# Kernel tuning notes

Hardware: AMD Instinct MI355X
Metric: run time of the kernel (lower is better)

## Reference

```python
import jax, jax.numpy as jnp
import numpy as np

N_NODES = 100_000
N_EDGES = 1_200_000
D = 64


def setup_inputs() -> dict:
    key = jax.random.key(0)
    k1, k2, k3, k4, k5 = jax.random.split(key, 5)
    feat = jax.random.normal(k1, (N_NODES, D), dtype=jnp.float32)
    feat_0 = jax.random.normal(k2, (N_NODES, D), dtype=jnp.float32)
    std = 1.0 / np.sqrt(D)  # reset_parameters: uniform(-std, std), std = 1/sqrt(out_size)
    weight = jax.random.uniform(k3, (D, D), dtype=jnp.float32, minval=-std, maxval=std)
    src = jax.random.randint(k4, (N_EDGES,), 0, N_NODES, dtype=jnp.int32)
    dst = jax.random.randint(k5, (N_EDGES,), 0, N_NODES, dtype=jnp.int32)
    return {
        "feat": feat,
        "feat_0": feat_0,
        "weight": weight,
        "src": src,
        "dst": dst,
        "alpha": jnp.float32(0.1),
        "lamda": jnp.float32(0.5),
        "layer": 1,
    }


def reference(feat, feat_0, weight, src, dst, alpha, lamda, layer):
    # beta = log(lamda / layer + 1)
    beta = jnp.log(lamda / layer + 1.0)
    # in-degrees from destination endpoints, clamped at 1 (as in DGL path)
    degs = jax.ops.segment_sum(
        jnp.ones_like(dst, dtype=feat.dtype), dst, num_segments=N_NODES
    )
    norm = jnp.maximum(degs, 1.0) ** -0.5  # [N]
    norm = norm[:, None]  # [N, 1]
    # symmetric degree-normalized SpMM: D^{-1/2} A D^{-1/2} X via copy_u + sum
    h = feat * norm
    h = jax.ops.segment_sum(h[src], dst, num_segments=N_NODES)  # scatter-add over edges
    h = h * norm
    # GCNII combination: initial residual + identity mapping
    feat_sum = h * (1.0 - alpha) + feat_0 * alpha
    rst = (1.0 - beta) * feat_sum + beta * (feat_sum @ weight)
    return rst
```

## Files before the change

kernel.cpp:

```cpp
#include <hip/hip_runtime.h>

#define DDIM 64
#define MAXNS 2048
#define PART_TPB 256
#define PART_EPT 16
#define PART_EPB (PART_TPB * PART_EPT)

__device__ __forceinline__ float atomAddF(float* p, float v) {
    return unsafeAtomicAdd(p, v);
}


__global__ void slice_count_kernel(const int* __restrict__ dst, int* __restrict__ sliceCnt,
                                   int nE, int NS) {
    __shared__ int lh[MAXNS];
    int t = threadIdx.x;
    int blockBase = blockIdx.x * PART_EPB;
    for (int i = t; i < NS; i += PART_TPB) lh[i] = 0;
    __syncthreads();
    #pragma unroll
    for (int c = 0; c < 4; ++c) {
        int e0 = blockBase + (c * PART_TPB + t) * 4;
        if (e0 + 3 < nE) {
            int4 b = *(const int4*)(dst + e0);
            atomicAdd(&lh[b.x >> 8], 1); atomicAdd(&lh[b.y >> 8], 1);
            atomicAdd(&lh[b.z >> 8], 1); atomicAdd(&lh[b.w >> 8], 1);
        } else {
            for (int j = 0; j < 4; ++j) {
                int e = e0 + j;
                if (e < nE) atomicAdd(&lh[dst[e] >> 8], 1);
            }
        }
    }
    __syncthreads();
    for (int i = t; i < NS; i += PART_TPB)
        if (lh[i]) atomicAdd(&sliceCnt[i], lh[i]);
}

__global__ void slice_scan_wp_kernel(int* __restrict__ scnt, int* __restrict__ sbase,
                                     int NS, int nE,
                                     const float* __restrict__ W, const float* __restrict__ lamda_p,
                                     const int* __restrict__ layer_p, float* __restrict__ Wp) {
    __shared__ int sdata[512];
    int t = threadIdx.x;
    int base = t * 4;
    int v[4];
    #pragma unroll
    for (int j = 0; j < 4; ++j) {
        int idx = base + j;
        v[j] = (idx < NS) ? scnt[idx] : 0;
    }
    int local = v[0] + v[1] + v[2] + v[3];
    sdata[t] = local;
    __syncthreads();
    for (int off = 1; off < 512; off <<= 1) {
        int y = (t >= off) ? sdata[t - off] : 0;
        __syncthreads();
        sdata[t] += y;
        __syncthreads();
    }
    int run = sdata[t] - local;
    #pragma unroll
    for (int j = 0; j < 4; ++j) {
        int idx = base + j;
        if (idx < NS) { sbase[idx] = run; scnt[idx] = run; }
        run += v[j];
    }
    if (t == 0) sbase[NS] = nE;

    float lam = lamda_p[0];
    int lb = layer_p[0];
    float layerf = (lb > 0 && lb < (1 << 23)) ? (float)lb : __int_as_float(lb);
    float beta = logf(lam / layerf + 1.0f);
    for (int i = t; i < DDIM * DDIM; i += 512) {
        int k = i >> 6, d = i & 63;
        float w = beta * W[i];
        if (k == d) w += (1.0f - beta);
        Wp[i] = w;
    }
}

__global__ void partition_kernel(const int* __restrict__ src, const int* __restrict__ dst,
                                 int* __restrict__ cursor, unsigned* __restrict__ staging,
                                 int nE, int NS) {
    __shared__ int lh[MAXNS];
    __shared__ int lbase[MAXNS];
    int t = threadIdx.x;
    int blockBase = blockIdx.x * PART_EPB;
    for (int i = t; i < NS; i += PART_TPB) lh[i] = 0;
    __syncthreads();

    int se[PART_EPT]; int de[PART_EPT];
    #pragma unroll
    for (int c = 0; c < 4; ++c) {
        int e0 = blockBase + (c * PART_TPB + t) * 4;
        if (e0 + 3 < nE) {
            int4 a = *(const int4*)(src + e0);
            int4 b = *(const int4*)(dst + e0);
            se[4*c+0] = a.x; se[4*c+1] = a.y; se[4*c+2] = a.z; se[4*c+3] = a.w;
            de[4*c+0] = b.x; de[4*c+1] = b.y; de[4*c+2] = b.z; de[4*c+3] = b.w;
        } else {
            #pragma unroll
            for (int j = 0; j < 4; ++j) {
                int e = e0 + j;
                se[4*c+j] = (e < nE) ? src[e] : 0;
                de[4*c+j] = (e < nE) ? dst[e] : -1;
            }
        }
    }
    #pragma unroll
    for (int k = 0; k < PART_EPT; ++k)
        if (de[k] >= 0) atomicAdd(&lh[de[k] >> 8], 1);
    __syncthreads();
    for (int i = t; i < NS; i += PART_TPB) {
        int c = lh[i];
        if (c) lbase[i] = atomicAdd(&cursor[i], c);
        lh[i] = 0;
    }
    __syncthreads();
    #pragma unroll
    for (int k = 0; k < PART_EPT; ++k) {
        int d = de[k];
        if (d >= 0) {
            int sl = d >> 8;
            int off = atomicAdd(&lh[sl], 1);
            staging[lbase[sl] + off] = ((unsigned)se[k] << 8) | (unsigned)(d & 255);
        }
    }
}

__global__ void bin_fill_kernel(const unsigned* __restrict__ staging, const int* __restrict__ sbase,
                                int* __restrict__ degI, float* __restrict__ normv,
                                int* __restrict__ row_end, int* __restrict__ eidx, int nN) {
    __shared__ int cnt[256];
    __shared__ int pos[256];
    int s = blockIdx.x;
    int t = threadIdx.x;
    int b0 = sbase[s], b1 = sbase[s + 1];
    cnt[t] = 0;
    __syncthreads();
    for (int j = b0 + t; j < b1; j += 256) {
        unsigned p = staging[j];
        atomicAdd(&cnt[p & 255], 1);
    }
    __syncthreads();
    int c = cnt[t];
    pos[t] = c;
    __syncthreads();
    for (int off = 1; off < 256; off <<= 1) {
        int y = (t >= off) ? pos[t - off] : 0;
        __syncthreads();
        pos[t] += y;
        __syncthreads();
    }
    int inc = pos[t];
    int exc = inc - c;
    int node = (s << 8) + t;
    if (node < nN) {
        degI[node] = c;
        normv[node] = rsqrtf(fmaxf((float)c, 1.0f));
        row_end[node] = b0 + inc;
    }
    pos[t] = b0 + exc;
    __syncthreads();
    for (int j = b0 + t; j < b1; j += 256) {
        unsigned p = staging[j];
        int q = atomicAdd(&pos[p & 255], 1);
        eidx[q] = (int)(p >> 8);
    }
}

__global__ void scale_kernel(const float4* __restrict__ feat4, const float* __restrict__ normv,
                             float4* __restrict__ featS4, int nN) {
    int b = blockIdx.x, t = threadIdx.x;
    int node = b * 16 + (t >> 4);
    int r = t & 15;
    if (node < nN) {
        float nv = normv[node];
        float4 v = feat4[(size_t)node * 16 + r];
        v.x *= nv; v.y *= nv; v.z *= nv; v.w *= nv;
        featS4[(size_t)node * 16 + r] = v;
    }
}


__global__ void deg_int_kernel(const int* __restrict__ dst, int* __restrict__ degI, int nE) {
    int i = blockIdx.x * blockDim.x + threadIdx.x;
    int base = i * 4;
    if (base + 3 < nE) {
        int4 d = *(const int4*)(dst + base);
        atomicAdd(&degI[d.x], 1); atomicAdd(&degI[d.y], 1);
        atomicAdd(&degI[d.z], 1); atomicAdd(&degI[d.w], 1);
    } else {
        for (int j = base; j < nE; ++j) atomicAdd(&degI[dst[j]], 1);
    }
}

#define SCAN_BLOCK 256
#define SCAN_CHUNK 1024

__global__ void scan1_kernel(const int* __restrict__ degI, int* __restrict__ row_start,
                             float* __restrict__ normv, int* __restrict__ blockSums, int nN) {
    __shared__ int sdata[SCAN_BLOCK];
    int t = threadIdx.x;
    int base = blockIdx.x * SCAN_CHUNK + t * 4;
    int v[4];
    #pragma unroll
    for (int j = 0; j < 4; ++j) {
        int idx = base + j;
        v[j] = (idx < nN) ? degI[idx] : 0;
    }
    int local = v[0] + v[1] + v[2] + v[3];
    sdata[t] = local;
    __syncthreads();
    for (int off = 1; off < SCAN_BLOCK; off <<= 1) {
        int y = (t >= off) ? sdata[t - off] : 0;
        __syncthreads();
        sdata[t] += y;
        __syncthreads();
    }
    int inc = sdata[t];
    int exc = inc - local;
    if (t == SCAN_BLOCK - 1) blockSums[blockIdx.x] = inc;
    int run = exc;
    #pragma unroll
    for (int j = 0; j < 4; ++j) {
        int idx = base + j;
        if (idx < nN) {
            row_start[idx] = run;
            normv[idx] = rsqrtf(fmaxf((float)v[j], 1.0f));
        }
        run += v[j];
    }
}

__global__ void scan2_wp_kernel(int* __restrict__ blockSums, int nb,
                                const float* __restrict__ W, const float* __restrict__ lamda_p,
                                const int* __restrict__ layer_p, float* __restrict__ Wp) {
    __shared__ int sdata[SCAN_BLOCK];
    int t = threadIdx.x;
    int v = (t < nb) ? blockSums[t] : 0;
    sdata[t] = v;
    __syncthreads();
    for (int off = 1; off < SCAN_BLOCK; off <<= 1) {
        int y = (t >= off) ? sdata[t - off] : 0;
        __syncthreads();
        sdata[t] += y;
        __syncthreads();
    }
    if (t < nb) blockSums[t] = sdata[t] - v;

    float lam = lamda_p[0];
    int lb = layer_p[0];
    float layerf = (lb > 0 && lb < (1 << 23)) ? (float)lb : __int_as_float(lb);
    float beta = logf(lam / layerf + 1.0f);
    for (int i = t; i < DDIM * DDIM; i += SCAN_BLOCK) {
        int k = i >> 6, d = i & 63;
        float w = beta * W[i];
        if (k == d) w += (1.0f - beta);
        Wp[i] = w;
    }
}

__global__ void scan3_scale_kernel(int* __restrict__ row_start, const int* __restrict__ blockSums,
                                   const float4* __restrict__ feat4, const float* __restrict__ normv,
                                   float4* __restrict__ featS4, int nN) {
    int b = blockIdx.x, t = threadIdx.x;
    int node = b * 16 + (t >> 4);
    int r = t & 15;
    if (node < nN) {
        float nv = normv[node];
        float4 v = feat4[(size_t)node * 16 + r];
        v.x *= nv; v.y *= nv; v.z *= nv; v.w *= nv;
        featS4[(size_t)node * 16 + r] = v;
    }
    if (t < 16) {
        int n2 = b * 16 + t;
        if (n2 < nN) row_start[n2] += blockSums[n2 >> 10];
    }
}

__global__ void scan3_kernel(int* __restrict__ row_start, const int* __restrict__ blockSums, int nN) {
    int i = blockIdx.x * blockDim.x + threadIdx.x;
    if (i < nN) row_start[i] += blockSums[i >> 10];
}

__global__ void fill_kernel(const int* __restrict__ src, const int* __restrict__ dst,
                            int* __restrict__ row_start, int* __restrict__ eidx, int nE) {
    int i = blockIdx.x * blockDim.x + threadIdx.x;
    int base = i * 4;
    if (base + 3 < nE) {
        int4 s = *(const int4*)(src + base);
        int4 d = *(const int4*)(dst + base);
        eidx[atomicAdd(&row_start[d.x], 1)] = s.x;
        eidx[atomicAdd(&row_start[d.y], 1)] = s.y;
        eidx[atomicAdd(&row_start[d.z], 1)] = s.z;
        eidx[atomicAdd(&row_start[d.w], 1)] = s.w;
    } else {
        for (int j = base; j < nE; ++j) {
            int tt = dst[j];
            int p = atomicAdd(&row_start[tt], 1);
            eidx[p] = src[j];
        }
    }
}

template<bool SCALED>
__global__ void gather_kernel(const float4* __restrict__ featv, const float4* __restrict__ feat04,
                              const float* __restrict__ normv, const int* __restrict__ degI,
                              const int* __restrict__ row_end, const int* __restrict__ eidx,
                              const float* __restrict__ Wp, const float* __restrict__ alpha_p,
                              float4* __restrict__ out4, int nN) {
    __shared__ float4 sW[DDIM * 16];
    const float4* Wp4 = (const float4*)Wp;
    for (int i = threadIdx.x; i < DDIM * 16; i += blockDim.x) {
        sW[(i & ~15) | ((i & 15) ^ ((i >> 8) & 3))] = Wp4[i];
    }
    __syncthreads();

    int lane = threadIdx.x & 63;
    int w = threadIdx.x >> 6;
    int g = lane >> 4;
    int r = lane & 15;
    int n = blockIdx.x * 4 + w;
    if (n >= nN) return;

    int end = row_end[n];
    int deg = degI[n];
    int start = end - deg;

    float4 acc = make_float4(0.f, 0.f, 0.f, 0.f);

    for (int j0 = start; j0 < end; j0 += 64) {
        int m = end - j0; if (m > 64) m = 64;
        int sIdx = 0;
        float nv = 1.0f;
        if (lane < m) {
            sIdx = eidx[j0 + lane];
            if (!SCALED) nv = normv[sIdx];
        }
        int nt = (m + 3) >> 2;
        int t = 0;
        for (; t + 2 <= nt; t += 2) {
            int e0 = 4 * t + g, e1 = e0 + 4;
            int s0 = __shfl(sIdx, e0, 64);
            int s1 = __shfl(sIdx, e1, 64);
            float ns0 = SCALED ? 1.0f : __shfl(nv, e0, 64);
            float ns1 = SCALED ? 1.0f : __shfl(nv, e1, 64);
            float4 a = featv[(size_t)s0 * 16 + r];
            float4 b = featv[(size_t)s1 * 16 + r];
            float w0 = (e0 < m) ? ns0 : 0.0f;
            float w1 = (e1 < m) ? ns1 : 0.0f;
            acc.x = fmaf(a.x, w0, acc.x); acc.y = fmaf(a.y, w0, acc.y);
            acc.z = fmaf(a.z, w0, acc.z); acc.w = fmaf(a.w, w0, acc.w);
            acc.x = fmaf(b.x, w1, acc.x); acc.y = fmaf(b.y, w1, acc.y);
            acc.z = fmaf(b.z, w1, acc.z); acc.w = fmaf(b.w, w1, acc.w);
        }
        for (; t < nt; ++t) {
            int e = 4 * t + g;
            int s = __shfl(sIdx, e, 64);
            float ns = SCALED ? 1.0f : __shfl(nv, e, 64);
            float4 a = featv[(size_t)s * 16 + r];
            float w0 = (e < m) ? ns : 0.0f;
            acc.x = fmaf(a.x, w0, acc.x); acc.y = fmaf(a.y, w0, acc.y);
            acc.z = fmaf(a.z, w0, acc.z); acc.w = fmaf(a.w, w0, acc.w);
        }
    }

    acc.x += __shfl_xor(acc.x, 16, 64); acc.y += __shfl_xor(acc.y, 16, 64);
    acc.z += __shfl_xor(acc.z, 16, 64); acc.w += __shfl_xor(acc.w, 16, 64);
    acc.x += __shfl_xor(acc.x, 32, 64); acc.y += __shfl_xor(acc.y, 32, 64);
    acc.z += __shfl_xor(acc.z, 32, 64); acc.w += __shfl_xor(acc.w, 32, 64);

    float alpha = alpha_p[0];
    float sn = normv[n] * (1.0f - alpha);
    float4 f0 = feat04[(size_t)n * 16 + r];
    float4 fs;
    fs.x = fmaf(acc.x, sn, f0.x * alpha);
    fs.y = fmaf(acc.y, sn, f0.y * alpha);
    fs.z = fmaf(acc.z, sn, f0.z * alpha);
    fs.w = fmaf(acc.w, sn, f0.w * alpha);

    float4 res = make_float4(0.f, 0.f, 0.f, 0.f);
    #pragma unroll
    for (int kk = 0; kk < 16; ++kk) {
        int srcLane = 4 * g + (kk >> 2);
        float fscomp = ((kk & 3) == 0) ? fs.x : ((kk & 3) == 1) ? fs.y
                     : ((kk & 3) == 2) ? fs.z : fs.w;
        float fsk = __shfl(fscomp, srcLane, 64);
        float4 wv = sW[(16 * g + kk) * 16 + (r ^ g)];
        res.x = fmaf(fsk, wv.x, res.x);
        res.y = fmaf(fsk, wv.y, res.y);
        res.z = fmaf(fsk, wv.z, res.z);
        res.w = fmaf(fsk, wv.w, res.w);
    }
    res.x += __shfl_xor(res.x, 16, 64); res.y += __shfl_xor(res.y, 16, 64);
    res.z += __shfl_xor(res.z, 16, 64); res.w += __shfl_xor(res.w, 16, 64);
    res.x += __shfl_xor(res.x, 32, 64); res.y += __shfl_xor(res.y, 32, 64);
    res.z += __shfl_xor(res.z, 32, 64); res.w += __shfl_xor(res.w, 32, 64);

    if (g == 0) out4[(size_t)n * 16 + r] = res;
}


__global__ void deg_kernel(const int* __restrict__ dst, float* __restrict__ degs, int nE) {
    int i = blockIdx.x * blockDim.x + threadIdx.x;
    if (i < nE) atomAddF(&degs[dst[i]], 1.0f);
}

__global__ void norm_kernel(float* degs, int nN) {
    int i = blockIdx.x * blockDim.x + threadIdx.x;
    if (i < nN) degs[i] = rsqrtf(fmaxf(degs[i], 1.0f));
}

__global__ void wp_kernel(const float* __restrict__ W, const float* __restrict__ lamda_p,
                          const int* __restrict__ layer_p, float* __restrict__ Wp) {
    int i = blockIdx.x * blockDim.x + threadIdx.x;
    if (i < DDIM * DDIM) {
        float lam = lamda_p[0];
        int lb = layer_p[0];
        float layerf = (lb > 0 && lb < (1 << 23)) ? (float)lb : __int_as_float(lb);
        float beta = logf(lam / layerf + 1.0f);
        int k = i >> 6, d = i & 63;
        float w = beta * W[i];
        if (k == d) w += (1.0f - beta);
        Wp[i] = w;
    }
}

__global__ void scatter_kernel(const float* __restrict__ feat, const float* __restrict__ norm,
                               const int* __restrict__ src, const int* __restrict__ dst,
                               float* __restrict__ accum, int nE) {
    long long gid = (long long)blockIdx.x * blockDim.x + threadIdx.x;
    int e = (int)(gid >> 6);
    int d = (int)(gid & 63);
    if (e < nE) {
        int s = src[e];
        int t = dst[e];
        float v = feat[(size_t)s * DDIM + d] * norm[s];
        atomAddF(&accum[(size_t)t * DDIM + d], v);
    }
}

__global__ void final_kernel(float* __restrict__ out, const float* __restrict__ feat0,
                             const float* __restrict__ norm, const float* __restrict__ Wp,
                             const float* __restrict__ alpha_p, int nN) {
    __shared__ float sW[DDIM * DDIM];
    for (int i = threadIdx.x; i < DDIM * DDIM; i += blockDim.x) sW[i] = Wp[i];
    __syncthreads();
    float alpha = alpha_p[0];
    int lane = threadIdx.x & 63;
    int w = threadIdx.x >> 6;
    int wavesPerBlock = blockDim.x >> 6;
    int nGroups = (nN + wavesPerBlock - 1) / wavesPerBlock;
    for (int gi = blockIdx.x; gi < nGroups; gi += gridDim.x) {
        int n = gi * wavesPerBlock + w;
        bool valid = n < nN;
        float fs = 0.0f;
        if (valid) {
            fs = out[(size_t)n * DDIM + lane] * norm[n] * (1.0f - alpha)
               + feat0[(size_t)n * DDIM + lane] * alpha;
        }
        float acc = 0.0f;
        #pragma unroll
        for (int k = 0; k < DDIM; ++k) {
            float fsk = __shfl(fs, k, 64);
            acc = fmaf(fsk, sW[k * DDIM + lane], acc);
        }
        if (valid) out[(size_t)n * DDIM + lane] = acc;
    }
}


static inline size_t align256(size_t x) { return (x + 255) & ~(size_t)255; }

extern "C" void kernel_launch(void* const* d_in, const int* in_sizes, int n_in,
                              void* d_out, int out_size, void* d_ws, size_t ws_size,
                              hipStream_t stream) {
    const float* feat  = (const float*)d_in[0];
    const float* feat0 = (const float*)d_in[1];
    const float* W     = (const float*)d_in[2];
    const int*   src   = (const int*)d_in[3];
    const int*   dst   = (const int*)d_in[4];
    const float* alpha = (const float*)d_in[5];
    const float* lamda = (const float*)d_in[6];
    const int*   layer = (const int*)d_in[7];
    float* out = (float*)d_out;

    int nN = in_sizes[0] / DDIM;
    int nE = in_sizes[3];
    int NS = (nN + 255) >> 8;
    int nb = (nN + SCAN_CHUNK - 1) / SCAN_CHUNK;

    size_t off = 0;
    size_t o_degI  = off; off += align256((size_t)nN * 4);
    size_t o_norm  = off; off += align256((size_t)nN * 4);
    size_t o_rowe  = off; off += align256((size_t)nN * 4);
    size_t o_sbase = off; off += align256((size_t)(NS + 1) * 4);
    size_t o_scnt  = off; off += align256((size_t)NS * 4);
    size_t o_wp    = off; off += align256((size_t)DDIM * DDIM * 4);
    size_t o_eidx  = off; off += align256((size_t)nE * 4);
    size_t base_sz = off;
    size_t o_featS = off; off += align256((size_t)nN * DDIM * 4);
    size_t need_t1 = off;
    size_t o_stag2 = base_sz;
    size_t need_t2 = base_sz + align256((size_t)nE * 4);

    bool newok = (NS >= 1 && NS <= MAXNS && nN <= (1 << 24));
    bool t1ok  = newok && ws_size >= need_t1 && ((size_t)nE * 4 <= (size_t)nN * DDIM * 4);
    bool t2ok  = newok && ws_size >= need_t2;

    if (t1ok || t2ok) {
        int*      degI  = (int*)  ((char*)d_ws + o_degI);
        float*    normv = (float*)((char*)d_ws + o_norm);
        int*      rowe  = (int*)  ((char*)d_ws + o_rowe);
        int*      sbase = (int*)  ((char*)d_ws + o_sbase);
        int*      scnt  = (int*)  ((char*)d_ws + o_scnt);
        float*    Wp    = (float*)((char*)d_ws + o_wp);
        int*      eidx  = (int*)  ((char*)d_ws + o_eidx);
        unsigned* stag  = (unsigned*)((char*)d_ws + (t1ok ? o_featS : o_stag2));
        float*    featS = (float*)((char*)d_ws + o_featS);

        hipMemsetAsync(scnt, 0, (size_t)NS * 4, stream);
        int pblocks = (nE + PART_EPB - 1) / PART_EPB;
        if (pblocks < 1) pblocks = 1;
        slice_count_kernel<<<pblocks, PART_TPB, 0, stream>>>(dst, scnt, nE, NS);
        slice_scan_wp_kernel<<<1, 512, 0, stream>>>(scnt, sbase, NS, nE, W, lamda, layer, Wp);
        partition_kernel<<<pblocks, PART_TPB, 0, stream>>>(src, dst, scnt, stag, nE, NS);
        bin_fill_kernel<<<NS, 256, 0, stream>>>(stag, sbase, degI, normv, rowe, eidx, nN);

        int gblocks = (nN + 3) / 4;
        if (t1ok) {
            scale_kernel<<<(nN + 15) / 16, 256, 0, stream>>>(
                (const float4*)feat, normv, (float4*)featS, nN);
            gather_kernel<true><<<gblocks, 256, 0, stream>>>(
                (const float4*)featS, (const float4*)feat0, normv, degI, rowe, eidx,
                Wp, alpha, (float4*)out, nN);
        } else {
            gather_kernel<false><<<gblocks, 256, 0, stream>>>(
                (const float4*)feat, (const float4*)feat0, normv, degI, rowe, eidx,
                Wp, alpha, (float4*)out, nN);
        }
        return;
    }

    off = 0;
    size_t f_degI = off;      off += align256((size_t)nN * 4);
    size_t f_norm = off;      off += align256((size_t)nN * 4);
    size_t f_rows = off;      off += align256((size_t)nN * 4);
    size_t f_bsum = off;      off += align256((size_t)nb * 4);
    size_t f_wp   = off;      off += align256((size_t)DDIM * DDIM * 4);
    size_t f_eidx = off;      off += align256((size_t)nE * 4);
    size_t need_csr = off;
    size_t f_featS = off;     off += align256((size_t)nN * DDIM * 4);
    size_t need_full = off;

    if (ws_size >= need_csr && nb <= SCAN_BLOCK) {
        int*   degI  = (int*)  ((char*)d_ws + f_degI);
        float* normv = (float*)((char*)d_ws + f_norm);
        int*   rows  = (int*)  ((char*)d_ws + f_rows);
        int*   bsum  = (int*)  ((char*)d_ws + f_bsum);
        float* Wp    = (float*)((char*)d_ws + f_wp);
        int*   eidx  = (int*)  ((char*)d_ws + f_eidx);
        bool scaled = (ws_size >= need_full);
        float* featS = (float*)((char*)d_ws + f_featS);

        hipMemsetAsync(degI, 0, (size_t)nN * 4, stream);
        int e4blocks = ((nE + 3) / 4 + 255) / 256;
        deg_int_kernel<<<e4blocks, 256, 0, stream>>>(dst, degI, nE);
        scan1_kernel<<<nb, SCAN_BLOCK, 0, stream>>>(degI, rows, normv, bsum, nN);
        scan2_wp_kernel<<<1, SCAN_BLOCK, 0, stream>>>(bsum, nb, W, lamda, layer, Wp);
        if (scaled) {
            scan3_scale_kernel<<<(nN + 15) / 16, 256, 0, stream>>>(
                rows, bsum, (const float4*)feat, normv, (float4*)featS, nN);
        } else {
            scan3_kernel<<<(nN + 255) / 256, 256, 0, stream>>>(rows, bsum, nN);
        }
        fill_kernel<<<e4blocks, 256, 0, stream>>>(src, dst, rows, eidx, nE);

        int gblocks = (nN + 3) / 4;
        if (scaled) {
            gather_kernel<true><<<gblocks, 256, 0, stream>>>(
                (const float4*)featS, (const float4*)feat0, normv, degI, rows, eidx,
                Wp, alpha, (float4*)out, nN);
        } else {
            gather_kernel<false><<<gblocks, 256, 0, stream>>>(
                (const float4*)feat, (const float4*)feat0, normv, degI, rows, eidx,
                Wp, alpha, (float4*)out, nN);
        }
    } else {
        float* degs = (float*)d_ws;
        size_t degs_bytes_al = align256((size_t)nN * 4);
        float* Wp = (float*)((char*)d_ws + degs_bytes_al);

        hipMemsetAsync(out, 0, (size_t)out_size * sizeof(float), stream);
        hipMemsetAsync(degs, 0, (size_t)nN * sizeof(float), stream);

        deg_kernel<<<(nE + 255) / 256, 256, 0, stream>>>(dst, degs, nE);
        norm_kernel<<<(nN + 255) / 256, 256, 0, stream>>>(degs, nN);
        wp_kernel<<<(DDIM * DDIM + 255) / 256, 256, 0, stream>>>(W, lamda, layer, Wp);

        long long tot = (long long)nE * DDIM;
        int sblocks = (int)((tot + 255) / 256);
        scatter_kernel<<<sblocks, 256, 0, stream>>>(feat, degs, src, dst, out, nE);
        final_kernel<<<2048, 256, 0, stream>>>(out, feat0, degs, Wp, alpha, nN);
    }
}
```

Baseline: 135.1 us.

## Store pre-scaled features in fp16 and make gather grid-stride persistent

```diff
diff --git a/kernel.cpp b/kernel.cpp
--- a/kernel.cpp
+++ b/kernel.cpp
@@ -1,4 +1,5 @@
 #include <hip/hip_runtime.h>
+#include <hip/hip_fp16.h>
 
 #define DDIM 64
 #define MAXNS 2048
@@ -171,15 +172,19 @@
 }
 
 __global__ void scale_kernel(const float4* __restrict__ feat4, const float* __restrict__ normv,
-                             float4* __restrict__ featS4, int nN) {
+                             uint2* __restrict__ featS2, int nN) {
     int b = blockIdx.x, t = threadIdx.x;
     int node = b * 16 + (t >> 4);
     int r = t & 15;
     if (node < nN) {
         float nv = normv[node];
         float4 v = feat4[(size_t)node * 16 + r];
-        v.x *= nv; v.y *= nv; v.z *= nv; v.w *= nv;
-        featS4[(size_t)node * 16 + r] = v;
+        __half2 h0 = __floats2half2_rn(v.x * nv, v.y * nv);
+        __half2 h1 = __floats2half2_rn(v.z * nv, v.w * nv);
+        uint2 u;
+        u.x = *(unsigned*)&h0;
+        u.y = *(unsigned*)&h1;
+        featS2[(size_t)node * 16 + r] = u;
     }
 }
 
@@ -264,15 +269,19 @@
 
 __global__ void scan3_scale_kernel(int* __restrict__ row_start, const int* __restrict__ blockSums,
                                    const float4* __restrict__ feat4, const float* __restrict__ normv,
-                                   float4* __restrict__ featS4, int nN) {
+                                   uint2* __restrict__ featS2, int nN) {
     int b = blockIdx.x, t = threadIdx.x;
     int node = b * 16 + (t >> 4);
     int r = t & 15;
     if (node < nN) {
         float nv = normv[node];
         float4 v = feat4[(size_t)node * 16 + r];
-        v.x *= nv; v.y *= nv; v.z *= nv; v.w *= nv;
-        featS4[(size_t)node * 16 + r] = v;
+        __half2 h0 = __floats2half2_rn(v.x * nv, v.y * nv);
+        __half2 h1 = __floats2half2_rn(v.z * nv, v.w * nv);
+        uint2 u;
+        u.x = *(unsigned*)&h0;
+        u.y = *(unsigned*)&h1;
+        featS2[(size_t)node * 16 + r] = u;
     }
     if (t < 16) {
         int n2 = b * 16 + t;
@@ -305,8 +314,8 @@
     }
 }
 
-template<bool SCALED>
-__global__ void gather_kernel(const float4* __restrict__ featv, const float4* __restrict__ feat04,
+template<bool HALF>
+__global__ void gather_kernel(const void* __restrict__ featv_, const float4* __restrict__ feat04,
                               const float* __restrict__ normv, const int* __restrict__ degI,
                               const int* __restrict__ row_end, const int* __restrict__ eidx,
                               const float* __restrict__ Wp, const float* __restrict__ alpha_p,
@@ -318,88 +327,114 @@
     }
     __syncthreads();
 
+    const float4* featF = (const float4*)featv_;
+    const uint2*  featH = (const uint2*)featv_;
+
     int lane = threadIdx.x & 63;
     int w = threadIdx.x >> 6;
     int g = lane >> 4;
     int r = lane & 15;
-    int n = blockIdx.x * 4 + w;
-    if (n >= nN) return;
-
-    int end = row_end[n];
-    int deg = degI[n];
-    int start = end - deg;
-
-    float4 acc = make_float4(0.f, 0.f, 0.f, 0.f);
-
-    for (int j0 = start; j0 < end; j0 += 64) {
-        int m = end - j0; if (m > 64) m = 64;
-        int sIdx = 0;
-        float nv = 1.0f;
-        if (lane < m) {
-            sIdx = eidx[j0 + lane];
-            if (!SCALED) nv = normv[sIdx];
-        }
-        int nt = (m + 3) >> 2;
-        int t = 0;
-        for (; t + 2 <= nt; t += 2) {
-            int e0 = 4 * t + g, e1 = e0 + 4;
-            int s0 = __shfl(sIdx, e0, 64);
-            int s1 = __shfl(sIdx, e1, 64);
-            float ns0 = SCALED ? 1.0f : __shfl(nv, e0, 64);
-            float ns1 = SCALED ? 1.0f : __shfl(nv, e1, 64);
-            float4 a = featv[(size_t)s0 * 16 + r];
-            float4 b = featv[(size_t)s1 * 16 + r];
-            float w0 = (e0 < m) ? ns0 : 0.0f;
-            float w1 = (e1 < m) ? ns1 : 0.0f;
-            acc.x = fmaf(a.x, w0, acc.x); acc.y = fmaf(a.y, w0, acc.y);
-            acc.z = fmaf(a.z, w0, acc.z); acc.w = fmaf(a.w, w0, acc.w);
-            acc.x = fmaf(b.x, w1, acc.x); acc.y = fmaf(b.y, w1, acc.y);
-            acc.z = fmaf(b.z, w1, acc.z); acc.w = fmaf(b.w, w1, acc.w);
-        }
-        for (; t < nt; ++t) {
-            int e = 4 * t + g;
-            int s = __shfl(sIdx, e, 64);
-            float ns = SCALED ? 1.0f : __shfl(nv, e, 64);
-            float4 a = featv[(size_t)s * 16 + r];
-            float w0 = (e < m) ? ns : 0.0f;
-            acc.x = fmaf(a.x, w0, acc.x); acc.y = fmaf(a.y, w0, acc.y);
-            acc.z = fmaf(a.z, w0, acc.z); acc.w = fmaf(a.w, w0, acc.w);
-        }
-    }
-
-    acc.x += __shfl_xor(acc.x, 16, 64); acc.y += __shfl_xor(acc.y, 16, 64);
-    acc.z += __shfl_xor(acc.z, 16, 64); acc.w += __shfl_xor(acc.w, 16, 64);
-    acc.x += __shfl_xor(acc.x, 32, 64); acc.y += __shfl_xor(acc.y, 32, 64);
-    acc.z += __shfl_xor(acc.z, 32, 64); acc.w += __shfl_xor(acc.w, 32, 64);
-
     float alpha = alpha_p[0];
-    float sn = normv[n] * (1.0f - alpha);
-    float4 f0 = feat04[(size_t)n * 16 + r];
-    float4 fs;
-    fs.x = fmaf(acc.x, sn, f0.x * alpha);
-    fs.y = fmaf(acc.y, sn, f0.y * alpha);
-    fs.z = fmaf(acc.z, sn, f0.z * alpha);
-    fs.w = fmaf(acc.w, sn, f0.w * alpha);
-
-    float4 res = make_float4(0.f, 0.f, 0.f, 0.f);
-    #pragma unroll
-    for (int kk = 0; kk < 16; ++kk) {
-        int srcLane = 4 * g + (kk >> 2);
-        float fscomp = ((kk & 3) == 0) ? fs.x : ((kk & 3) == 1) ? fs.y
-                     : ((kk & 3) == 2) ? fs.z : fs.w;
-        float fsk = __shfl(fscomp, srcLane, 64);
-        float4 wv = sW[(16 * g + kk) * 16 + (r ^ g)];
-        res.x = fmaf(fsk, wv.x, res.x);
-        res.y = fmaf(fsk, wv.y, res.y);
-        res.z = fmaf(fsk, wv.z, res.z);
-        res.w = fmaf(fsk, wv.w, res.w);
-    }
-    res.x += __shfl_xor(res.x, 16, 64); res.y += __shfl_xor(res.y, 16, 64);
-    res.z += __shfl_xor(res.z, 16, 64); res.w += __shfl_xor(res.w, 16, 64);
-    res.x += __shfl_xor(res.x, 32, 64); res.y += __shfl_xor(res.y, 32, 64);
-    res.z += __shfl_xor(res.z, 32, 64); res.w += __shfl_xor(res.w, 32, 64);
-
-    if (g == 0) out4[(size_t)n * 16 + r] = res;
+
+    for (int n = blockIdx.x * 4 + w; n < nN; n += gridDim.x * 4) {
+        int end = row_end[n];
+        int deg = degI[n];
+        int start = end - deg;
+
+        float4 acc = make_float4(0.f, 0.f, 0.f, 0.f);
+
+        for (int j0 = start; j0 < end; j0 += 64) {
+            int m = end - j0; if (m > 64) m = 64;
+            int sIdx = 0;
+            float nv = 1.0f;
+            if (lane < m) {
+                sIdx = eidx[j0 + lane];
+                if (!HALF) nv = normv[sIdx];
+            }
+            int nt = (m + 3) >> 2;
+            int t = 0;
+            for (; t + 2 <= nt; t += 2) {
+                int e0 = 4 * t + g, e1 = e0 + 4;
+                int s0 = __shfl(sIdx, e0, 64);
+                int s1 = __shfl(sIdx, e1, 64);
+                float w0 = (e0 < m) ? 1.0f : 0.0f;
+                float w1 = (e1 < m) ? 1.0f : 0.0f;
+                if (HALF) {
+                    uint2 ua = featH[(size_t)s0 * 16 + r];
+                    uint2 ub = featH[(size_t)s1 * 16 + r];
+                    float2 a0 = __half22float2(*(const __half2*)&ua.x);
+                    float2 a1 = __half22float2(*(const __half2*)&ua.y);
+                    float2 b0 = __half22float2(*(const __half2*)&ub.x);
+                    float2 b1 = __half22float2(*(const __half2*)&ub.y);
+                    acc.x = fmaf(a0.x, w0, acc.x); acc.y = fmaf(a0.y, w0, acc.y);
+                    acc.z = fmaf(a1.x, w0, acc.z); acc.w = fmaf(a1.y, w0, acc.w);
+                    acc.x = fmaf(b0.x, w1, acc.x); acc.y = fmaf(b0.y, w1, acc.y);
+                    acc.z = fmaf(b1.x, w1, acc.z); acc.w = fmaf(b1.y, w1, acc.w);
+                } else {
+                    float ns0 = __shfl(nv, e0, 64);
+                    float ns1 = __shfl(nv, e1, 64);
+                    w0 *= ns0; w1 *= ns1;
+                    float4 a = featF[(size_t)s0 * 16 + r];
+                    float4 b = featF[(size_t)s1 * 16 + r];
+                    acc.x = fmaf(a.x, w0, acc.x); acc.y = fmaf(a.y, w0, acc.y);
+                    acc.z = fmaf(a.z, w0, acc.z); acc.w = fmaf(a.w, w0, acc.w);
+                    acc.x = fmaf(b.x, w1, acc.x); acc.y = fmaf(b.y, w1, acc.y);
+                    acc.z = fmaf(b.z, w1, acc.z); acc.w = fmaf(b.w, w1, acc.w);
+                }
+            }
+            for (; t < nt; ++t) {
+                int e = 4 * t + g;
+                int s = __shfl(sIdx, e, 64);
+                float w0 = (e < m) ? 1.0f : 0.0f;
+                if (HALF) {
+                    uint2 ua = featH[(size_t)s * 16 + r];
+                    float2 a0 = __half22float2(*(const __half2*)&ua.x);
+                    float2 a1 = __half22float2(*(const __half2*)&ua.y);
+                    acc.x = fmaf(a0.x, w0, acc.x); acc.y = fmaf(a0.y, w0, acc.y);
+                    acc.z = fmaf(a1.x, w0, acc.z); acc.w = fmaf(a1.y, w0, acc.w);
+                } else {
+                    float ns = __shfl(nv, e, 64);
+                    w0 *= ns;
+                    float4 a = featF[(size_t)s * 16 + r];
+                    acc.x = fmaf(a.x, w0, acc.x); acc.y = fmaf(a.y, w0, acc.y);
+                    acc.z = fmaf(a.z, w0, acc.z); acc.w = fmaf(a.w, w0, acc.w);
+                }
+            }
+        }
+
+        acc.x += __shfl_xor(acc.x, 16, 64); acc.y += __shfl_xor(acc.y, 16, 64);
+        acc.z += __shfl_xor(acc.z, 16, 64); acc.w += __shfl_xor(acc.w, 16, 64);
+        acc.x += __shfl_xor(acc.x, 32, 64); acc.y += __shfl_xor(acc.y, 32, 64);
+        acc.z += __shfl_xor(acc.z, 32, 64); acc.w += __shfl_xor(acc.w, 32, 64);
+
+        float sn = normv[n] * (1.0f - alpha);
+        float4 f0 = feat04[(size_t)n * 16 + r];
+        float4 fs;
+        fs.x = fmaf(acc.x, sn, f0.x * alpha);
+        fs.y = fmaf(acc.y, sn, f0.y * alpha);
+        fs.z = fmaf(acc.z, sn, f0.z * alpha);
+        fs.w = fmaf(acc.w, sn, f0.w * alpha);
+
+        float4 res = make_float4(0.f, 0.f, 0.f, 0.f);
+        #pragma unroll
+        for (int kk = 0; kk < 16; ++kk) {
+            int srcLane = 4 * g + (kk >> 2);
+            float fscomp = ((kk & 3) == 0) ? fs.x : ((kk & 3) == 1) ? fs.y
+                         : ((kk & 3) == 2) ? fs.z : fs.w;
+            float fsk = __shfl(fscomp, srcLane, 64);
+            float4 wv = sW[(16 * g + kk) * 16 + (r ^ g)];
+            res.x = fmaf(fsk, wv.x, res.x);
+            res.y = fmaf(fsk, wv.y, res.y);
+            res.z = fmaf(fsk, wv.z, res.z);
+            res.w = fmaf(fsk, wv.w, res.w);
+        }
+        res.x += __shfl_xor(res.x, 16, 64); res.y += __shfl_xor(res.y, 16, 64);
+        res.z += __shfl_xor(res.z, 16, 64); res.w += __shfl_xor(res.w, 16, 64);
+        res.x += __shfl_xor(res.x, 32, 64); res.y += __shfl_xor(res.y, 32, 64);
+        res.z += __shfl_xor(res.z, 32, 64); res.w += __shfl_xor(res.w, 32, 64);
+
+        if (g == 0) out4[(size_t)n * 16 + r] = res;
+    }
 }
 
 
@@ -501,13 +536,13 @@
     size_t o_wp    = off; off += align256((size_t)DDIM * DDIM * 4);
     size_t o_eidx  = off; off += align256((size_t)nE * 4);
     size_t base_sz = off;
-    size_t o_featS = off; off += align256((size_t)nN * DDIM * 4);
+    size_t o_featS = off; off += align256((size_t)nN * DDIM * 2);
     size_t need_t1 = off;
     size_t o_stag2 = base_sz;
     size_t need_t2 = base_sz + align256((size_t)nE * 4);
 
-    bool newok = (NS >= 1 && NS <= MAXNS && nN <= (1 << 24));
-    bool t1ok  = newok && ws_size >= need_t1 && ((size_t)nE * 4 <= (size_t)nN * DDIM * 4);
+    bool newok = (NS >= 1 && NS <= MAXNS && nN <= (1 << 23));
+    bool t1ok  = newok && ws_size >= need_t1 && ((size_t)nE * 4 <= (size_t)nN * DDIM * 2);
     bool t2ok  = newok && ws_size >= need_t2;
 
     if (t1ok || t2ok) {
@@ -530,15 +565,16 @@
         bin_fill_kernel<<<NS, 256, 0, stream>>>(stag, sbase, degI, normv, rowe, eidx, nN);
 
         int gblocks = (nN + 3) / 4;
+        if (gblocks > 4096) gblocks = 4096;
         if (t1ok) {
             scale_kernel<<<(nN + 15) / 16, 256, 0, stream>>>(
-                (const float4*)feat, normv, (float4*)featS, nN);
+                (const float4*)feat, normv, (uint2*)featS, nN);
             gather_kernel<true><<<gblocks, 256, 0, stream>>>(
-                (const float4*)featS, (const float4*)feat0, normv, degI, rowe, eidx,
+                (const void*)featS, (const float4*)feat0, normv, degI, rowe, eidx,
                 Wp, alpha, (float4*)out, nN);
         } else {
             gather_kernel<false><<<gblocks, 256, 0, stream>>>(
-                (const float4*)feat, (const float4*)feat0, normv, degI, rowe, eidx,
+                (const void*)feat, (const float4*)feat0, normv, degI, rowe, eidx,
                 Wp, alpha, (float4*)out, nN);
         }
         return;
@@ -552,7 +588,7 @@
     size_t f_wp   = off;      off += align256((size_t)DDIM * DDIM * 4);
     size_t f_eidx = off;      off += align256((size_t)nE * 4);
     size_t need_csr = off;
-    size_t f_featS = off;     off += align256((size_t)nN * DDIM * 4);
+    size_t f_featS = off;     off += align256((size_t)nN * DDIM * 2);
     size_t need_full = off;
 
     if (ws_size >= need_csr && nb <= SCAN_BLOCK) {
@@ -572,20 +608,21 @@
         scan2_wp_kernel<<<1, SCAN_BLOCK, 0, stream>>>(bsum, nb, W, lamda, layer, Wp);
         if (scaled) {
             scan3_scale_kernel<<<(nN + 15) / 16, 256, 0, stream>>>(
-                rows, bsum, (const float4*)feat, normv, (float4*)featS, nN);
+                rows, bsum, (const float4*)feat, normv, (uint2*)featS, nN);
         } else {
             scan3_kernel<<<(nN + 255) / 256, 256, 0, stream>>>(rows, bsum, nN);
         }
         fill_kernel<<<e4blocks, 256, 0, stream>>>(src, dst, rows, eidx, nE);
 
         int gblocks = (nN + 3) / 4;
+        if (gblocks > 4096) gblocks = 4096;
         if (scaled) {
             gather_kernel<true><<<gblocks, 256, 0, stream>>>(
-                (const float4*)featS, (const float4*)feat0, normv, degI, rows, eidx,
+                (const void*)featS, (const float4*)feat0, normv, degI, rows, eidx,
                 Wp, alpha, (float4*)out, nN);
         } else {
             gather_kernel<false><<<gblocks, 256, 0, stream>>>(
-                (const float4*)feat, (const float4*)feat0, normv, degI, rows, eidx,
+                (const void*)feat, (const float4*)feat0, normv, degI, rows, eidx,
                 Wp, alpha, (float4*)out, nN);
         }
     } else {
```

Measured after the change: 132.9 us. No clear change (-1.6%).
